# Optimization experiments

Hardware: AMD Instinct MI355X
Metric: run time of the kernel (lower is better)

The kernel has to match this reference:

```python
import jax, jax.numpy as jnp
import numpy as np

N, E, HID, H, L, EF = 50000, 640000, 128, 8, 3, 16
C = HID // H  # 16, per-head output channels (concat=True)
NEG_SLOPE = 0.2
LN_EPS = 1e-5


def setup_inputs() -> dict:
    key = jax.random.key(0)
    ks = jax.random.split(key, 12)
    s = 0.05
    x = jax.random.normal(ks[0], (N, HID), jnp.float32)
    batch_index = jnp.sort(jax.random.randint(ks[1], (N,), 0, 64, dtype=jnp.int32))
    edge_index = jax.random.randint(ks[2], (2, E), 0, N, dtype=jnp.int32)
    edge_attr = jax.random.normal(ks[3], (E, EF), jnp.float32)
    # edge_transform: Linear(EF, HID)
    Wt = jax.random.normal(ks[4], (EF, HID), jnp.float32) * s
    bt = jnp.zeros((HID,), jnp.float32)
    # per-layer GATv2 params (stacked over L layers)
    Wl = jax.random.normal(ks[5], (L, HID, HID), jnp.float32) * s  # lin_l (source)
    bl = jnp.zeros((L, HID), jnp.float32)
    Wr = jax.random.normal(ks[6], (L, HID, HID), jnp.float32) * s  # lin_r (target)
    br = jnp.zeros((L, HID), jnp.float32)
    We = jax.random.normal(ks[7], (L, HID, HID), jnp.float32) * s  # lin_edge (no bias)
    att = jax.random.normal(ks[8], (L, H, C), jnp.float32) * s
    bias_o = jnp.zeros((L, HID), jnp.float32)
    ln_g = jnp.ones((L, HID), jnp.float32)
    ln_b = jnp.zeros((L, HID), jnp.float32)
    return dict(x=x, batch_index=batch_index, edge_index=edge_index, edge_attr=edge_attr,
                Wt=Wt, bt=bt, Wl=Wl, bl=bl, Wr=Wr, br=br, We=We, att=att,
                bias_o=bias_o, ln_g=ln_g, ln_b=ln_b)


def _layer_norm(x, g, b):
    mu = jnp.mean(x, axis=-1, keepdims=True)
    var = jnp.var(x, axis=-1, keepdims=True)
    return g * (x - mu) * jax.lax.rsqrt(var + LN_EPS) + b


def _gatv2_layer(x, ea, src, dst, Wl, bl, Wr, br, We, att, bias_o):
    # node transforms: lin_l for source features, lin_r for target features
    xl = (x @ Wl + bl).reshape(N, H, C)
    xr = (x @ Wr + br).reshape(N, H, C)
    em = (ea @ We).reshape(E, H, C)
    # per-edge attention logits (GATv2: leaky_relu AFTER the sum, then dot with att)
    m = jax.nn.leaky_relu(xl[src] + xr[dst] + em, NEG_SLOPE)  # [E,H,C]
    logits = jnp.einsum('ehc,hc->eh', m, att)                  # [E,H]
    # segment softmax over incoming edges of each destination node
    lmax = jax.ops.segment_max(logits, dst, num_segments=N)    # [N,H]
    p = jnp.exp(logits - lmax[dst])
    denom = jax.ops.segment_sum(p, dst, num_segments=N)        # [N,H]
    alpha = p / (denom[dst] + 1e-16)
    # weighted scatter-aggregate of source messages
    out = jax.ops.segment_sum(xl[src] * alpha[:, :, None], dst, num_segments=N)  # [N,H,C]
    return out.reshape(N, HID) + bias_o


def reference(x, batch_index, edge_index, edge_attr, Wt, bt, Wl, bl, Wr, br, We, att, bias_o, ln_g, ln_b):
    src, dst = edge_index[0], edge_index[1]
    ea = edge_attr @ Wt + bt  # shared edge_transform, [E,HID]
    for l in range(L):
        out = _gatv2_layer(x, ea, src, dst, Wl[l], bl[l], Wr[l], br[l], We[l], att[l], bias_o[l])
        out = _layer_norm(out, ln_g[l], ln_b[l])
        x = jax.nn.relu(out) + x  # dropout p=0 -> identity; residual
    return x
```

## Files before the change

kernel.cpp:

```cpp
#include <hip/hip_runtime.h>

#define N_NODES 50000
#define N_EDGES 640000
#define HID 128
#define EF 16
#define NLAYERS 3
#define CHUNK 16
#define SCAN_BLOCKS 196

typedef __attribute__((ext_vector_type(8))) short short8;
typedef __attribute__((ext_vector_type(8))) _Float16 half8;
typedef __attribute__((ext_vector_type(4))) float f32x4;
typedef __attribute__((ext_vector_type(2))) float f32x2;

__device__ __forceinline__ unsigned short f2bf(float f) {
  unsigned int u = __float_as_uint(f);
  u = u + 0x7FFFu + ((u >> 16) & 1u);
  return (unsigned short)(u >> 16);
}

__device__ __forceinline__ unsigned short f2h(float f) {
  _Float16 h = (_Float16)f;
  return *(unsigned short*)&h;
}

__device__ __forceinline__ float dpp_hadd8(float v) {
  int x;
  x = __builtin_amdgcn_update_dpp(0, __float_as_int(v), 0xB1, 0xF, 0xF, true);
  v += __int_as_float(x);
  x = __builtin_amdgcn_update_dpp(0, __float_as_int(v), 0x4E, 0xF, 0xF, true);
  v += __int_as_float(x);
  x = __builtin_amdgcn_update_dpp(0, __float_as_int(v), 0x141, 0xF, 0xF, true);
  v += __int_as_float(x);
  return v;
}

__device__ __forceinline__ f32x2 pk_add(f32x2 a, f32x2 b) {
  f32x2 d;
  asm("v_pk_add_f32 %0, %1, %2" : "=v"(d) : "v"(a), "v"(b));
  return d;
}
__device__ __forceinline__ f32x2 pk_mul(f32x2 a, f32x2 b) {
  f32x2 d;
  asm("v_pk_mul_f32 %0, %1, %2" : "=v"(d) : "v"(a), "v"(b));
  return d;
}

__device__ __forceinline__ int pslot(int j) {
  return (((j >> 4) * 8 + (j & 7)) << 1) + ((j >> 3) & 1);
}

__global__ __launch_bounds__(256) void k_setup(const float* __restrict__ Wt,
                                               const float* __restrict__ bt,
                                               const float* __restrict__ We,
                                               const float* __restrict__ Wl,
                                               const float* __restrict__ Wr,
                                               const float* __restrict__ x,
                                               const int* __restrict__ dst,
                                               int* __restrict__ counts,
                                               float* __restrict__ ct,
                                               unsigned short* __restrict__ MtB,
                                               unsigned short* __restrict__ WT,
                                               unsigned short* __restrict__ xbf) {
  int b = blockIdx.x, t = threadIdx.x;
  if (b < 26) {
    int id = b * 256 + t;
    const int total = NLAYERS * (EF + 1) * HID;
    if (id >= total) return;
    int l = id / ((EF + 1) * HID);
    int r = id % ((EF + 1) * HID);
    int row = r / HID;
    int j = r % HID;
    const float* Wel = We + l * HID * HID;
    float s = 0.f;
    if (row < EF) {
      const float* wtr = Wt + row * HID;
      for (int i = 0; i < HID; ++i) s += wtr[i] * Wel[i * HID + j];
      int blk = j >> 4, nn = j & 15;
      size_t base = (size_t)(l * 8 + blk) * 64;
      MtB[(base + (size_t)((row >> 3) * 16 + nn)) * 8 + (row & 7)] = f2h(s);
      MtB[(base + (size_t)((2 + (row >> 3)) * 16 + nn)) * 8 + (row & 7)] = 0;
    } else {
      for (int i = 0; i < HID; ++i) s += bt[i] * Wel[i * HID + j];
      ct[l * HID + pslot(j)] = s;
    }
  } else if (b < 410) {
    int id = (b - 26) * 256 + t;
    int k = id & (HID - 1);
    int n = (id >> 7) & (HID - 1);
    int s = (id >> 14) & 1;
    int l = id >> 15;
    const float* W = (s == 0 ? Wl : Wr) + (size_t)l * HID * HID;
    WT[id] = f2bf(W[k * HID + n]);
  } else if (b < 3535) {
    int id = (b - 410) * 256 + t;
    const float4* p = (const float4*)(x + (size_t)id * 8);
    float4 a = p[0], bb = p[1];
    unsigned short o[8] = {f2bf(a.x), f2bf(a.y), f2bf(a.z), f2bf(a.w),
                           f2bf(bb.x), f2bf(bb.y), f2bf(bb.z), f2bf(bb.w)};
    *(uint4*)(xbf + (size_t)id * 8) = *(uint4*)o;
  } else {
    int e = (b - 3535) * 256 + t;
    if (e < N_EDGES) atomicAdd(&counts[dst[e]], 1);
  }
}

__global__ __launch_bounds__(256) void k_scan1(const int* __restrict__ counts,
                                               int* __restrict__ rowptr,
                                               int* __restrict__ bsum) {
  __shared__ int sc[256];
  int t = threadIdx.x;
  int i = blockIdx.x * 256 + t;
  int v = (i < N_NODES) ? counts[i] : 0;
  sc[t] = v;
  __syncthreads();
  for (int off = 1; off < 256; off <<= 1) {
    int u = 0;
    if (t >= off) u = sc[t - off];
    __syncthreads();
    sc[t] += u;
    __syncthreads();
  }
  if (i < N_NODES) rowptr[i] = sc[t] - v;
  if (t == 255) bsum[blockIdx.x] = sc[255];
}

__global__ __launch_bounds__(256) void k_scan2(int* __restrict__ bsum) {
  __shared__ int sc[256];
  int t = threadIdx.x;
  int v = (t < SCAN_BLOCKS) ? bsum[t] : 0;
  sc[t] = v;
  __syncthreads();
  for (int off = 1; off < 256; off <<= 1) {
    int u = 0;
    if (t >= off) u = sc[t - off];
    __syncthreads();
    sc[t] += u;
    __syncthreads();
  }
  bsum[t] = sc[t] - v;
}

__global__ __launch_bounds__(256) void k_scan3(int* __restrict__ rowptr, const int* __restrict__ bsum) {
  int t = threadIdx.x;
  int i = blockIdx.x * 256 + t;
  if (i < N_NODES) rowptr[i] += bsum[blockIdx.x];
  if (i == 0) rowptr[N_NODES] = N_EDGES;
}

__global__ __launch_bounds__(256) void k_fill(const int* __restrict__ src,
                                              const int* __restrict__ dst,
                                              const int* __restrict__ rowptr,
                                              int* __restrict__ fill,
                                              int* __restrict__ ssrc,
                                              const float* __restrict__ eattr,
                                              unsigned short* __restrict__ eaA) {
  int e = blockIdx.x * 256 + threadIdx.x;
  if (e >= N_EDGES) return;
  int d = dst[e];
  int pos = atomicAdd(&fill[d], 1);
  int idx = rowptr[d] + pos;
  ssrc[idx] = src[e] << 6;
  const float* pe = eattr + (size_t)e * EF;
  unsigned short* po = eaA + (size_t)idx * 16;
#pragma unroll
  for (int g = 0; g < 2; ++g) {
    unsigned short o[8];
#pragma unroll
    for (int k = 0; k < 8; ++k) o[k] = f2h(pe[g * 8 + k]);
    *(uint4*)(po + g * 8) = *(uint4*)o;
  }
}

__global__ __launch_bounds__(256) void k_gemm_mfma(const unsigned short* __restrict__ xbf,
                                                   const unsigned short* __restrict__ WTl,
                                                   const float* __restrict__ bl,
                                                   const float* __restrict__ br,
                                                   const float* __restrict__ ctl,
                                                   unsigned short* __restrict__ xlb,
                                                   unsigned short* __restrict__ xrb) {
  __shared__ short As[64 * 136];
  __shared__ short Bs[128 * 136];
  int t = threadIdx.x;
  int s = blockIdx.y;
  int row0 = blockIdx.x * 64;

  const uint4* gx = (const uint4*)xbf;
#pragma unroll
  for (int p = 0; p < 4; ++p) {
    int c = t + p * 256;
    int row = c >> 4, col16 = c & 15;
    int grow = row0 + row;
    if (grow >= N_NODES) grow = N_NODES - 1;
    uint4 v = gx[grow * 16 + col16];
    *(uint4*)(&As[row * 136 + col16 * 8]) = v;
  }
  const uint4* gw = (const uint4*)WTl;
#pragma unroll
  for (int p = 0; p < 8; ++p) {
    int c = t + p * 256;
    int row = c >> 4, col16 = c & 15;
    uint4 v = gw[s * 2048 + row * 16 + col16];
    *(uint4*)(&Bs[row * 136 + col16 * 8]) = v;
  }
  __syncthreads();

  int lane = t & 63, w = t >> 6;
  int quad = lane >> 4, lm = lane & 15;
  f32x4 acc[4][2];
#pragma unroll
  for (int mf = 0; mf < 4; ++mf)
#pragma unroll
    for (int nf = 0; nf < 2; ++nf) acc[mf][nf] = (f32x4)(0.f);

#pragma unroll
  for (int ks = 0; ks < 4; ++ks) {
    short8 af[4], bf[2];
#pragma unroll
    for (int mf = 0; mf < 4; ++mf)
      af[mf] = *(short8*)(&As[(mf * 16 + lm) * 136 + ks * 32 + quad * 8]);
#pragma unroll
    for (int nf = 0; nf < 2; ++nf)
      bf[nf] = *(short8*)(&Bs[(w * 32 + nf * 16 + lm) * 136 + ks * 32 + quad * 8]);
#pragma unroll
    for (int mf = 0; mf < 4; ++mf)
#pragma unroll
      for (int nf = 0; nf < 2; ++nf)
        acc[mf][nf] = __builtin_amdgcn_mfma_f32_16x16x32_bf16(af[mf], bf[nf], acc[mf][nf], 0, 0, 0);
  }

  const float* bias = (s == 0) ? bl : br;
  unsigned short* out = (s == 0) ? xlb : xrb;
#pragma unroll
  for (int nf = 0; nf < 2; ++nf) {
    int n = w * 32 + nf * 16 + lm;
    int slot = pslot(n);
    float bv = bias[n] + ((s == 1) ? ctl[slot] : 0.f);
#pragma unroll
    for (int mf = 0; mf < 4; ++mf) {
#pragma unroll
      for (int r = 0; r < 4; ++r) {
        int grow = row0 + mf * 16 + quad * 4 + r;
        if (grow < N_NODES) out[(size_t)grow * HID + slot] = f2bf(acc[mf][nf][r] + bv);
      }
    }
  }
}

__global__ __launch_bounds__(64) void k_fused(const float* __restrict__ xin,
                                              const unsigned int* __restrict__ xlb,
                                              const unsigned int* __restrict__ xrb,
                                              const int* __restrict__ rowptr,
                                              const int* __restrict__ ssrc,
                                              const unsigned short* __restrict__ eaA,
                                              const unsigned int* __restrict__ MtBl,
                                              const float* __restrict__ att,
                                              const float* __restrict__ bias_o,
                                              const float* __restrict__ lng,
                                              const float* __restrict__ lnb,
                                              float* __restrict__ xout,
                                              unsigned short* __restrict__ xbf_out) {
  __shared__ __align__(16) float em_s[CHUNK * 130];
  int n = blockIdx.x;
  int l = threadIdx.x;
  int lm = l & 15, quad = l >> 4;
  int j0 = (l >> 3) * 16 + (l & 7), j1 = j0 + 8;

  uint4 bfr[8];
  const uint4* mb = (const uint4*)MtBl;
#pragma unroll
  for (int b = 0; b < 8; ++b) bfr[b] = mb[b * 64 + l];

  unsigned int ur = xrb[(size_t)n * 64 + l];
  f32x2 base;
  base.x = __uint_as_float(ur << 16);
  base.y = __uint_as_float(ur & 0xFFFF0000u);
  const float LOG2E = 1.44269504088896340736f;
  f32x2 attp = {att[j0] * LOG2E, att[j1] * LOG2E};
  f32x2 c02 = {0.2f, 0.2f};
  int beg = rowptr[n], end = rowptr[n + 1];

  f32x2 acc = {0.f, 0.f};
  float denom = 0.f;

  half8 afz;
#pragma unroll
  for (int e2 = 0; e2 < 8; ++e2) afz[e2] = (_Float16)0.f;
  int sv = ssrc[beg + l];
  half8 af = afz;
  if (quad < 2) af = *(const half8*)(eaA + (size_t)(beg + lm) * 16 + quad * 8);

  for (int c0 = beg; c0 < end; c0 += CHUNK) {
    int cnt = min(CHUNK, end - c0);
    int sv_n = ssrc[c0 + CHUNK + l];
    half8 af_n = afz;
    if (quad < 2) af_n = *(const half8*)(eaA + (size_t)(c0 + CHUNK + lm) * 16 + quad * 8);

    f32x4 cc[8];
#pragma unroll
    for (int b = 0; b < 8; ++b)
      cc[b] = __builtin_amdgcn_mfma_f32_16x16x32_f16(af, *(half8*)&bfr[b], (f32x4)(0.f), 0, 0, 0);
#pragma unroll
    for (int b = 0; b < 8; ++b)
#pragma unroll
      for (int r = 0; r < 4; ++r)
        em_s[(quad * 4 + r) * 130 + ((b * 8 + (lm & 7)) << 1) + (lm >> 3)] = cc[b][r];

    auto srow = [&](int i) {
      return xlb + (unsigned int)__builtin_amdgcn_readlane(sv, i);
    };

    auto edge = [&](int i, unsigned int u) {
      f32x2 xls;
      xls.x = __uint_as_float(u << 16);
      xls.y = __uint_as_float(u & 0xFFFF0000u);
      f32x2 em = *(const f32x2*)(&em_s[i * 130 + 2 * l]);
      f32x2 m = pk_add(pk_add(base, xls), em);
      f32x2 ms = pk_mul(c02, m);
      m.x = fmaxf(m.x, ms.x);
      m.y = fmaxf(m.y, ms.y);
      f32x2 v2 = pk_mul(m, attp);
      float vs = dpp_hadd8(v2.x + v2.y);
      float p = exp2f(vs);
      denom += p;
      acc.x = fmaf(xls.x, p, acc.x);
      acc.y = fmaf(xls.y, p, acc.y);
    };

    unsigned int cur[4];
#pragma unroll
    for (int q = 0; q < 4; ++q) cur[q] = srow(q)[l];
    int cnt4 = cnt & ~3;
    for (int i = 0; i < cnt4; i += 4) {
      unsigned int nxt[4];
#pragma unroll
      for (int q = 0; q < 4; ++q) nxt[q] = srow(i + 4 + q)[l];
#pragma unroll
      for (int q = 0; q < 4; ++q) edge(i + q, cur[q]);
#pragma unroll
      for (int q = 0; q < 4; ++q) cur[q] = nxt[q];
    }
#pragma unroll
    for (int q = 0; q < 4; ++q)
      if (cnt4 + q < cnt) edge(cnt4 + q, cur[q]);

    sv = sv_n;
    af = af_n;
  }

  f32x2 outp;
  float inv = 1.f / (denom + 1e-16f);
  outp.x = acc.x * inv + bias_o[j0];
  outp.y = acc.y * inv + bias_o[j1];
  float s1 = outp.x + outp.y;
  float s2 = outp.x * outp.x + outp.y * outp.y;
#pragma unroll
  for (int mask = 1; mask <= 32; mask <<= 1) {
    s1 += __shfl_xor(s1, mask);
    s2 += __shfl_xor(s2, mask);
  }
  float mu = s1 * (1.f / 128.f);
  float var = s2 * (1.f / 128.f) - mu * mu;
  float rs = rsqrtf(var + 1e-5f);
  float y0 = lng[j0] * (outp.x - mu) * rs + lnb[j0];
  float y1 = lng[j1] * (outp.y - mu) * rs + lnb[j1];
  float r0 = fmaxf(y0, 0.f) + xin[(size_t)n * HID + j0];
  float r1 = fmaxf(y1, 0.f) + xin[(size_t)n * HID + j1];
  xout[(size_t)n * HID + j0] = r0;
  xout[(size_t)n * HID + j1] = r1;
  xbf_out[(size_t)n * HID + j0] = f2bf(r0);
  xbf_out[(size_t)n * HID + j1] = f2bf(r1);
}

extern "C" void kernel_launch(void* const* d_in, const int* in_sizes, int n_in,
                              void* d_out, int out_size, void* d_ws, size_t ws_size,
                              hipStream_t stream) {
  const float* x0    = (const float*)d_in[0];
  const int*   eidx  = (const int*)d_in[2];
  const float* eattr = (const float*)d_in[3];
  const float* Wt    = (const float*)d_in[4];
  const float* bt    = (const float*)d_in[5];
  const float* Wl    = (const float*)d_in[6];
  const float* bl    = (const float*)d_in[7];
  const float* Wr    = (const float*)d_in[8];
  const float* br    = (const float*)d_in[9];
  const float* We    = (const float*)d_in[10];
  const float* att   = (const float*)d_in[11];
  const float* bo    = (const float*)d_in[12];
  const float* lng   = (const float*)d_in[13];
  const float* lnb   = (const float*)d_in[14];
  float* out = (float*)d_out;
  const int* src = eidx;
  const int* dst = eidx + N_EDGES;

  char* ws = (char*)d_ws;
  size_t off = 0;
  auto alloc = [&](size_t bytes) {
    char* p = ws + off;
    off += (bytes + 255) & ~(size_t)255;
    return p;
  };
  int* counts = (int*)alloc((size_t)N_NODES * 4);
  int* fill   = (int*)alloc((size_t)N_NODES * 4);
  float* ct   = (float*)alloc((size_t)NLAYERS * HID * 4);
  int* rowptr = (int*)alloc((size_t)(N_NODES + 1) * 4);
  int* bsum   = (int*)alloc(256 * 4);
  int* ssrc   = (int*)alloc(((size_t)N_EDGES + 128) * 4);
  unsigned short* eaA = (unsigned short*)alloc(((size_t)N_EDGES + 32) * 16 * 2);
  unsigned short* MtB = (unsigned short*)alloc((size_t)NLAYERS * 8 * 64 * 8 * 2);
  unsigned short* xlb = (unsigned short*)alloc((size_t)N_NODES * HID * 2);
  unsigned short* xrb = (unsigned short*)alloc((size_t)N_NODES * HID * 2);
  float* xbuf = (float*)alloc((size_t)N_NODES * HID * 4);
  unsigned short* xbf = (unsigned short*)alloc((size_t)N_NODES * HID * 2);
  unsigned short* WTb = (unsigned short*)alloc((size_t)NLAYERS * 2 * HID * HID * 2);

  hipMemsetAsync(counts, 0, (char*)(fill + N_NODES) - (char*)counts, stream);
  hipMemsetAsync(ssrc + N_EDGES, 0, 128 * 4, stream);

  hipLaunchKernelGGL(k_setup, dim3(6035), dim3(256), 0, stream,
                     Wt, bt, We, Wl, Wr, x0, dst, counts, ct, MtB, WTb, xbf);
  hipLaunchKernelGGL(k_scan1, dim3(SCAN_BLOCKS), dim3(256), 0, stream, counts, rowptr, bsum);
  hipLaunchKernelGGL(k_scan2, dim3(1), dim3(256), 0, stream, bsum);
  hipLaunchKernelGGL(k_scan3, dim3(SCAN_BLOCKS), dim3(256), 0, stream, rowptr, bsum);
  hipLaunchKernelGGL(k_fill, dim3((N_EDGES + 255) / 256), dim3(256), 0, stream,
                     src, dst, rowptr, fill, ssrc, eattr, eaA);

  for (int l = 0; l < NLAYERS; ++l) {
    const float* xin = (l == 0) ? x0 : (const float*)xbuf;
    float* xout = (l == NLAYERS - 1) ? out : xbuf;
    hipLaunchKernelGGL(k_gemm_mfma, dim3((N_NODES + 63) / 64, 2), dim3(256), 0, stream,
                       xbf, WTb + (size_t)l * 2 * HID * HID, bl + l * HID, br + l * HID,
                       ct + (size_t)l * HID, xlb, xrb);
    hipLaunchKernelGGL(k_fused, dim3(N_NODES), dim3(64), 0, stream,
                       xin, (const unsigned int*)xlb, (const unsigned int*)xrb,
                       rowptr, ssrc, eaA,
                       (const unsigned int*)(MtB + (size_t)l * 8 * 64 * 8),
                       att + l * HID,
                       bo + l * HID, lng + l * HID, lnb + l * HID, xout, xbf);
  }
}
```

Before: 419.4 us.

## Reuse count atomics for CSR fill, merge GEMM halves, skip final bf16 write

The atomic position returned while counting in-degrees is now stored per edge and reused by the fill kernel, so the second atomic pass and the fill array go away. The GEMM now computes both the lin_l and lin_r outputs in one block, loading the activation tile once instead of twice. The fused kernel only prefetches the next chunk when one exists. It also skips writing bf16 activations on the last layer. These changes add an E-sized order buffer and more serial work per GEMM block in exchange for fewer atomics and less redundant traffic.

```diff
diff --git a/kernel.cpp b/kernel.cpp
--- a/kernel.cpp
+++ b/kernel.cpp
@@ -58,6 +58,7 @@
                                                const float* __restrict__ x,
                                                const int* __restrict__ dst,
                                                int* __restrict__ counts,
+                                               int* __restrict__ eord,
                                                float* __restrict__ ct,
                                                unsigned short* __restrict__ MtB,
                                                unsigned short* __restrict__ WT,
@@ -101,7 +102,10 @@
     *(uint4*)(xbf + (size_t)id * 8) = *(uint4*)o;
   } else {
     int e = (b - 3535) * 256 + t;
-    if (e < N_EDGES) atomicAdd(&counts[dst[e]], 1);
+    if (e < N_EDGES) {
+      int pos = atomicAdd(&counts[dst[e]], 1);
+      eord[e] = pos;
+    }
   }
 }
 
@@ -151,15 +155,14 @@
 __global__ __launch_bounds__(256) void k_fill(const int* __restrict__ src,
                                               const int* __restrict__ dst,
                                               const int* __restrict__ rowptr,
-                                              int* __restrict__ fill,
+                                              const int* __restrict__ eord,
                                               int* __restrict__ ssrc,
                                               const float* __restrict__ eattr,
                                               unsigned short* __restrict__ eaA) {
   int e = blockIdx.x * 256 + threadIdx.x;
   if (e >= N_EDGES) return;
   int d = dst[e];
-  int pos = atomicAdd(&fill[d], 1);
-  int idx = rowptr[d] + pos;
+  int idx = rowptr[d] + eord[e];
   ssrc[idx] = src[e] << 6;
   const float* pe = eattr + (size_t)e * EF;
   unsigned short* po = eaA + (size_t)idx * 16;
@@ -182,7 +185,6 @@
   __shared__ short As[64 * 136];
   __shared__ short Bs[128 * 136];
   int t = threadIdx.x;
-  int s = blockIdx.y;
   int row0 = blockIdx.x * 64;
 
   const uint4* gx = (const uint4*)xbf;
@@ -195,53 +197,58 @@
     uint4 v = gx[grow * 16 + col16];
     *(uint4*)(&As[row * 136 + col16 * 8]) = v;
   }
-  const uint4* gw = (const uint4*)WTl;
-#pragma unroll
-  for (int p = 0; p < 8; ++p) {
-    int c = t + p * 256;
-    int row = c >> 4, col16 = c & 15;
-    uint4 v = gw[s * 2048 + row * 16 + col16];
-    *(uint4*)(&Bs[row * 136 + col16 * 8]) = v;
-  }
-  __syncthreads();
 
   int lane = t & 63, w = t >> 6;
   int quad = lane >> 4, lm = lane & 15;
-  f32x4 acc[4][2];
-#pragma unroll
-  for (int mf = 0; mf < 4; ++mf)
-#pragma unroll
-    for (int nf = 0; nf < 2; ++nf) acc[mf][nf] = (f32x4)(0.f);
-
-#pragma unroll
-  for (int ks = 0; ks < 4; ++ks) {
-    short8 af[4], bf[2];
+  const uint4* gw = (const uint4*)WTl;
+
+  for (int s = 0; s < 2; ++s) {
+    if (s) __syncthreads();
+#pragma unroll
+    for (int p = 0; p < 8; ++p) {
+      int c = t + p * 256;
+      int row = c >> 4, col16 = c & 15;
+      uint4 v = gw[s * 2048 + row * 16 + col16];
+      *(uint4*)(&Bs[row * 136 + col16 * 8]) = v;
+    }
+    __syncthreads();
+
+    f32x4 acc[4][2];
 #pragma unroll
     for (int mf = 0; mf < 4; ++mf)
-      af[mf] = *(short8*)(&As[(mf * 16 + lm) * 136 + ks * 32 + quad * 8]);
-#pragma unroll
-    for (int nf = 0; nf < 2; ++nf)
-      bf[nf] = *(short8*)(&Bs[(w * 32 + nf * 16 + lm) * 136 + ks * 32 + quad * 8]);
-#pragma unroll
-    for (int mf = 0; mf < 4; ++mf)
+#pragma unroll
+      for (int nf = 0; nf < 2; ++nf) acc[mf][nf] = (f32x4)(0.f);
+
+#pragma unroll
+    for (int ks = 0; ks < 4; ++ks) {
+      short8 af[4], bf[2];
+#pragma unroll
+      for (int mf = 0; mf < 4; ++mf)
+        af[mf] = *(short8*)(&As[(mf * 16 + lm) * 136 + ks * 32 + quad * 8]);
 #pragma unroll
       for (int nf = 0; nf < 2; ++nf)
-        acc[mf][nf] = __builtin_amdgcn_mfma_f32_16x16x32_bf16(af[mf], bf[nf], acc[mf][nf], 0, 0, 0);
-  }
-
-  const float* bias = (s == 0) ? bl : br;
-  unsigned short* out = (s == 0) ? xlb : xrb;
-#pragma unroll
-  for (int nf = 0; nf < 2; ++nf) {
-    int n = w * 32 + nf * 16 + lm;
-    int slot = pslot(n);
-    float bv = bias[n] + ((s == 1) ? ctl[slot] : 0.f);
-#pragma unroll
-    for (int mf = 0; mf < 4; ++mf) {
-#pragma unroll
-      for (int r = 0; r < 4; ++r) {
-        int grow = row0 + mf * 16 + quad * 4 + r;
-        if (grow < N_NODES) out[(size_t)grow * HID + slot] = f2bf(acc[mf][nf][r] + bv);
+        bf[nf] = *(short8*)(&Bs[(w * 32 + nf * 16 + lm) * 136 + ks * 32 + quad * 8]);
+#pragma unroll
+      for (int mf = 0; mf < 4; ++mf)
+#pragma unroll
+        for (int nf = 0; nf < 2; ++nf)
+          acc[mf][nf] = __builtin_amdgcn_mfma_f32_16x16x32_bf16(af[mf], bf[nf], acc[mf][nf], 0, 0, 0);
+    }
+
+    const float* bias = (s == 0) ? bl : br;
+    unsigned short* out = (s == 0) ? xlb : xrb;
+#pragma unroll
+    for (int nf = 0; nf < 2; ++nf) {
+      int n = w * 32 + nf * 16 + lm;
+      int slot = pslot(n);
+      float bv = bias[n] + ((s == 1) ? ctl[slot] : 0.f);
+#pragma unroll
+      for (int mf = 0; mf < 4; ++mf) {
+#pragma unroll
+        for (int r = 0; r < 4; ++r) {
+          int grow = row0 + mf * 16 + quad * 4 + r;
+          if (grow < N_NODES) out[(size_t)grow * HID + slot] = f2bf(acc[mf][nf][r] + bv);
+        }
       }
     }
   }
@@ -292,9 +299,13 @@
 
   for (int c0 = beg; c0 < end; c0 += CHUNK) {
     int cnt = min(CHUNK, end - c0);
-    int sv_n = ssrc[c0 + CHUNK + l];
-    half8 af_n = afz;
-    if (quad < 2) af_n = *(const half8*)(eaA + (size_t)(c0 + CHUNK + lm) * 16 + quad * 8);
+    int sv_n = sv;
+    half8 af_n = af;
+    if (c0 + CHUNK < end) {
+      sv_n = ssrc[c0 + CHUNK + l];
+      af_n = afz;
+      if (quad < 2) af_n = *(const half8*)(eaA + (size_t)(c0 + CHUNK + lm) * 16 + quad * 8);
+    }
 
     f32x4 cc[8];
 #pragma unroll
@@ -368,8 +379,10 @@
   float r1 = fmaxf(y1, 0.f) + xin[(size_t)n * HID + j1];
   xout[(size_t)n * HID + j0] = r0;
   xout[(size_t)n * HID + j1] = r1;
-  xbf_out[(size_t)n * HID + j0] = f2bf(r0);
-  xbf_out[(size_t)n * HID + j1] = f2bf(r1);
+  if (xbf_out) {
+    xbf_out[(size_t)n * HID + j0] = f2bf(r0);
+    xbf_out[(size_t)n * HID + j1] = f2bf(r1);
+  }
 }
 
 extern "C" void kernel_launch(void* const* d_in, const int* in_sizes, int n_in,
@@ -401,7 +414,7 @@
     return p;
   };
   int* counts = (int*)alloc((size_t)N_NODES * 4);
-  int* fill   = (int*)alloc((size_t)N_NODES * 4);
+  int* eord   = (int*)alloc((size_t)N_EDGES * 4);
   float* ct   = (float*)alloc((size_t)NLAYERS * HID * 4);
   int* rowptr = (int*)alloc((size_t)(N_NODES + 1) * 4);
   int* bsum   = (int*)alloc(256 * 4);
@@ -414,21 +427,22 @@
   unsigned short* xbf = (unsigned short*)alloc((size_t)N_NODES * HID * 2);
   unsigned short* WTb = (unsigned short*)alloc((size_t)NLAYERS * 2 * HID * HID * 2);
 
-  hipMemsetAsync(counts, 0, (char*)(fill + N_NODES) - (char*)counts, stream);
+  hipMemsetAsync(counts, 0, (size_t)N_NODES * 4, stream);
   hipMemsetAsync(ssrc + N_EDGES, 0, 128 * 4, stream);
 
   hipLaunchKernelGGL(k_setup, dim3(6035), dim3(256), 0, stream,
-                     Wt, bt, We, Wl, Wr, x0, dst, counts, ct, MtB, WTb, xbf);
+                     Wt, bt, We, Wl, Wr, x0, dst, counts, eord, ct, MtB, WTb, xbf);
   hipLaunchKernelGGL(k_scan1, dim3(SCAN_BLOCKS), dim3(256), 0, stream, counts, rowptr, bsum);
   hipLaunchKernelGGL(k_scan2, dim3(1), dim3(256), 0, stream, bsum);
   hipLaunchKernelGGL(k_scan3, dim3(SCAN_BLOCKS), dim3(256), 0, stream, rowptr, bsum);
   hipLaunchKernelGGL(k_fill, dim3((N_EDGES + 255) / 256), dim3(256), 0, stream,
-                     src, dst, rowptr, fill, ssrc, eattr, eaA);
+                     src, dst, rowptr, eord, ssrc, eattr, eaA);
 
   for (int l = 0; l < NLAYERS; ++l) {
     const float* xin = (l == 0) ? x0 : (const float*)xbuf;
     float* xout = (l == NLAYERS - 1) ? out : xbuf;
-    hipLaunchKernelGGL(k_gemm_mfma, dim3((N_NODES + 63) / 64, 2), dim3(256), 0, stream,
+    unsigned short* xbf_next = (l == NLAYERS - 1) ? (unsigned short*)nullptr : xbf;
+    hipLaunchKernelGGL(k_gemm_mfma, dim3((N_NODES + 63) / 64), dim3(256), 0, stream,
                        xbf, WTb + (size_t)l * 2 * HID * HID, bl + l * HID, br + l * HID,
                        ct + (size_t)l * HID, xlb, xrb);
     hipLaunchKernelGGL(k_fused, dim3(N_NODES), dim3(64), 0, stream,
@@ -436,6 +450,6 @@
                        rowptr, ssrc, eaA,
                        (const unsigned int*)(MtB + (size_t)l * 8 * 64 * 8),
                        att + l * HID,
-                       bo + l * HID, lng + l * HID, lnb + l * HID, xout, xbf);
-  }
-}
+                       bo + l * HID, lng + l * HID, lnb + l * HID, xout, xbf_next);
+  }
+}
```

Measured after the change: 403.8 us. -3.7%, faster.
